# Performance work log

Measured on AMD Instinct MI355X. Metric: run time of the kernel, lower is better.

The kernel has to match this reference:

```python
import jax, jax.numpy as jnp
import numpy as np

D = 4096          # in_features == out_features (scale broadcast requires square W)
TOKENS = 16384


def setup_inputs() -> dict:
    key = jax.random.key(0)
    kx, kq, ks, kb = jax.random.split(key, 4)
    x = jax.random.normal(kx, (TOKENS, D), dtype=jnp.float32)
    # int4 quantized weights in [-8, 7] (stored int8 in torch; int32 here is fine)
    qweight = jax.random.randint(kq, (D, D), -8, 8, dtype=jnp.int32)
    # per-channel scales: positive, realistic magnitude ~ max|W|/7
    scale = jax.random.uniform(ks, (D,), dtype=jnp.float32, minval=1e-3, maxval=2e-2)
    bias = jax.random.normal(kb, (D,), dtype=jnp.float32)
    return {"x": x, "qweight": qweight, "scale": scale, "bias": bias}


def reference(x, qweight, scale, bias):
    # Dequantize: W[i, j] = qW[i, j] * scale[i]  (scale.view(-1,1) in the source)
    W = qweight.astype(jnp.float32) * scale[:, None]   # [out, in]
    # F.linear(x, W, bias) = x @ W.T + bias
    return x @ W.T + bias                               # [tokens, out]
```

## Files before the change

### kernel.cpp

```cpp
#include <hip/hip_runtime.h>

typedef __attribute__((ext_vector_type(4))) int  i8x16;
typedef __attribute__((ext_vector_type(16))) int i32x16;
typedef __attribute__((ext_vector_type(8))) short bf16x8;
typedef __attribute__((ext_vector_type(8))) unsigned short ushort8;
typedef __attribute__((ext_vector_type(4))) float f32x4;

__device__ __forceinline__ unsigned short f32_to_bf16(float f) {
    union { float f; unsigned int u; } v;
    v.f = f;
    unsigned int r = v.u + (0x7fffu + ((v.u >> 16) & 1u));
    return (unsigned short)(r >> 16);
}

__device__ __forceinline__ void gload_lds16(const void* g, void* l) {
    __builtin_amdgcn_global_load_lds(
        (const __attribute__((address_space(1))) unsigned int*)g,
        (__attribute__((address_space(3))) unsigned int*)l, 16, 0, 0);
}

__global__ __launch_bounds__(256) void quantx_kernel(const float* __restrict__ x,
                                                     char* __restrict__ xq,
                                                     float* __restrict__ rs, int K) {
    const int row = blockIdx.x;
    const float4* xr = (const float4*)(x + (size_t)row * K);
    const int K4 = K >> 2;
    const int t = threadIdx.x;
    float am = 0.f;
    for (int i = t; i < K4; i += 256) {
        float4 v = xr[i];
        am = fmaxf(am, fmaxf(fmaxf(fabsf(v.x), fabsf(v.y)),
                             fmaxf(fabsf(v.z), fabsf(v.w))));
    }
    for (int off = 32; off; off >>= 1) am = fmaxf(am, __shfl_xor(am, off));
    __shared__ float ws[4];
    if ((t & 63) == 0) ws[t >> 6] = am;
    __syncthreads();
    am = fmaxf(fmaxf(ws[0], ws[1]), fmaxf(ws[2], ws[3]));
    const float inv = am > 0.f ? 127.f / am : 0.f;
    if (t == 0) rs[row] = am > 0.f ? am / 127.f : 0.f;
    int* dst = (int*)(xq + (size_t)row * K);
    for (int i = t; i < K4; i += 256) {
        float4 v = xr[i];
        int a = (int)rintf(v.x * inv), b = (int)rintf(v.y * inv);
        int c = (int)rintf(v.z * inv), d = (int)rintf(v.w * inv);
        dst[i] = (a & 255) | ((b & 255) << 8) | ((c & 255) << 16) | (d << 24);
    }
}

__global__ void convq_kernel(const int* __restrict__ q, char* __restrict__ qb, long n16) {
    long i = (long)blockIdx.x * blockDim.x + threadIdx.x;
    const long stride = (long)gridDim.x * blockDim.x;
    for (; i < n16; i += stride) {
        const int4* p = (const int4*)(q + i * 16);
        int4 a = p[0], b = p[1], c = p[2], d = p[3];
        int4 r;
        r.x = (a.x & 255) | ((a.y & 255) << 8) | ((a.z & 255) << 16) | (a.w << 24);
        r.y = (b.x & 255) | ((b.y & 255) << 8) | ((b.z & 255) << 16) | (b.w << 24);
        r.z = (c.x & 255) | ((c.y & 255) << 8) | ((c.z & 255) << 16) | (c.w << 24);
        r.w = (d.x & 255) | ((d.y & 255) << 8) | ((d.z & 255) << 16) | (d.w << 24);
        ((int4*)qb)[i] = r;
    }
}

__global__ __launch_bounds__(512, 2) void qgemm_i8_kernel(
    const char* __restrict__ A, const char* __restrict__ B,
    const float* __restrict__ rs, const float* __restrict__ scale,
    const float* __restrict__ bias, float* __restrict__ C, int M, int N, int K) {
    extern __shared__ char sm[];

    const int tid  = threadIdx.x;
    const int lane = tid & 63;
    const int w    = tid >> 6;
    const int wr   = w >> 2;
    const int wc   = w & 3;
    const int l31  = lane & 31;
    const int hi   = lane >> 5;
    const int swz7 = l31 & 7;

    const int nwg = gridDim.x;
    const int bid = blockIdx.x;
    const int swz = (bid & 7) * (nwg >> 3) + (bid >> 3);
    const int nbx = N >> 8;
    const int m0  = (swz / nbx) << 8;
    const int n0  = (swz % nbx) << 8;

    const size_t binv0 = (size_t)(tid >> 3) * K +
                         (size_t)(((tid & 7) ^ ((tid >> 3) & 7)) << 4);
    const size_t bofs = (size_t)64 * K;
    const int bld = w << 10;

#define STAGE(LBASE, GSRC) do {                                       \
        gload_lds16((GSRC) + binv0,          (LBASE) + bld);          \
        gload_lds16((GSRC) + binv0 + bofs,   (LBASE) + bld + 8192);   \
        gload_lds16((GSRC) + binv0 + 2*bofs, (LBASE) + bld + 16384);  \
        gload_lds16((GSRC) + binv0 + 3*bofs, (LBASE) + bld + 24576); } while (0)

    const int aRow0 = (wr * 128 + l31) * 128;
    const int bRow0 = (wc * 64 + l31) * 128;

    const char* pA = A + (size_t)m0 * K;
    const char* pB = B + (size_t)n0 * K;
    const int NT = K >> 7;

    i32x16 acc[4][2];
#pragma unroll
    for (int mf = 0; mf < 4; ++mf)
#pragma unroll
        for (int nf = 0; nf < 2; ++nf)
#pragma unroll
            for (int r = 0; r < 16; ++r) acc[mf][nf][r] = 0;

#define RD_KH(BUFA, BUFB, KH) do {                                             \
    _Pragma("unroll") for (int mf = 0; mf < 4; ++mf)                           \
    _Pragma("unroll") for (int s = 0; s < 2; ++s)                              \
        aF[mf][s] = *(const i8x16*)((BUFA) + aRow0 + mf * 4096 +               \
            ((((KH) * 4 + s * 2 + hi) ^ swz7) << 4));                          \
    _Pragma("unroll") for (int nf = 0; nf < 2; ++nf)                           \
    _Pragma("unroll") for (int s = 0; s < 2; ++s)                              \
        bF[nf][s] = *(const i8x16*)((BUFB) + bRow0 + nf * 4096 +               \
            ((((KH) * 4 + s * 2 + hi) ^ swz7) << 4)); } while (0)
#define MFMA_KH() do {                                                         \
    _Pragma("unroll") for (int s = 0; s < 2; ++s)                              \
    _Pragma("unroll") for (int mf = 0; mf < 4; ++mf)                           \
    _Pragma("unroll") for (int nf = 0; nf < 2; ++nf)                           \
        acc[mf][nf] = __builtin_amdgcn_mfma_i32_32x32x32_i8(                   \
            aF[mf][s], bF[nf][s], acc[mf][nf], 0, 0, 0); } while (0)
#define LGKM0() do { asm volatile("s_waitcnt lgkmcnt(0)" ::: "memory");        \
                     __builtin_amdgcn_sched_barrier(0); } while (0)

    i8x16 aF[4][2], bF[2][2];

    STAGE(sm + 0,     pA);
    STAGE(sm + 65536, pB);
    if (NT > 1) {
        STAGE(sm + 32768, pA + 128);
        STAGE(sm + 98304, pB + 128);
        asm volatile("s_waitcnt vmcnt(8)" ::: "memory");
    } else {
        asm volatile("s_waitcnt vmcnt(0)" ::: "memory");
    }
    __builtin_amdgcn_s_barrier();

    for (int t = 0; t < NT; ++t) {
        char* Ac = sm + (t & 1) * 32768;
        char* Bc = sm + 65536 + (t & 1) * 32768;

        RD_KH(Ac, Bc, 0);
        LGKM0();
        __builtin_amdgcn_s_setprio(1);
        MFMA_KH();
        __builtin_amdgcn_s_setprio(0);

        RD_KH(Ac, Bc, 1);
        LGKM0();
        __builtin_amdgcn_s_setprio(1);
        MFMA_KH();
        __builtin_amdgcn_s_setprio(0);

        if (t + 1 < NT) {
            __builtin_amdgcn_s_barrier();
            if (t + 2 < NT) {
                STAGE(Ac, pA + (size_t)(t + 2) * 128);
                STAGE(Bc, pB + (size_t)(t + 2) * 128);
                asm volatile("s_waitcnt vmcnt(8)" ::: "memory");
            } else {
                asm volatile("s_waitcnt vmcnt(0)" ::: "memory");
            }
            __builtin_amdgcn_s_barrier();
        }
    }

#pragma unroll
    for (int mf = 0; mf < 4; ++mf) {
        const int rbase = m0 + wr * 128 + mf * 32 + 4 * hi;
#pragma unroll
        for (int nf = 0; nf < 2; ++nf) {
            const int col = n0 + wc * 64 + nf * 32 + l31;
            const float sc = scale[col];
            const float bs = bias[col];
#pragma unroll
            for (int reg = 0; reg < 16; ++reg) {
                const int row = rbase + 8 * (reg >> 2) + (reg & 3);
                C[(size_t)row * N + col] =
                    (float)acc[mf][nf][reg] * (rs[row] * sc) + bs;
            }
        }
    }
#undef STAGE
#undef RD_KH
#undef MFMA_KH
#undef LGKM0
}

__global__ __launch_bounds__(256) void qgemm_fb_kernel(
    const float* __restrict__ Af, const int* __restrict__ Bi,
    const float* __restrict__ scale, const float* __restrict__ bias,
    float* __restrict__ C, int M, int N, int K) {
    constexpr int BK = 64;
    __shared__ unsigned short lA[128 * BK];
    __shared__ unsigned short lB[128 * BK];
    const int t = threadIdx.x, lane = t & 63, w = t >> 6;
    const int wr = w >> 1, wc = w & 1;
    const int m0 = blockIdx.y * 128, n0 = blockIdx.x * 128;
    const int l15 = lane & 15, l4 = lane >> 4;
    f32x4 acc[4][4];
#pragma unroll
    for (int m = 0; m < 4; ++m)
#pragma unroll
        for (int n = 0; n < 4; ++n) acc[m][n] = (f32x4){0.f, 0.f, 0.f, 0.f};
    for (int k0 = 0; k0 < K; k0 += BK) {
        __syncthreads();
#pragma unroll
        for (int i = 0; i < 4; ++i) {
            const int off = i * 4096 + w * 1024 + lane * 16;
            const int row = off >> 7;
            const int col = (off & 127) >> 1;
            const float* pa = Af + (size_t)(m0 + row) * K + k0 + col;
            float4 a0 = *(const float4*)pa;
            float4 a1 = *(const float4*)(pa + 4);
            ushort8 va;
            va[0] = f32_to_bf16(a0.x); va[1] = f32_to_bf16(a0.y);
            va[2] = f32_to_bf16(a0.z); va[3] = f32_to_bf16(a0.w);
            va[4] = f32_to_bf16(a1.x); va[5] = f32_to_bf16(a1.y);
            va[6] = f32_to_bf16(a1.z); va[7] = f32_to_bf16(a1.w);
            *(ushort8*)((char*)lA + off) = va;
            const int* pb = Bi + (size_t)(n0 + row) * K + k0 + col;
            int4 b0 = *(const int4*)pb;
            int4 b1 = *(const int4*)(pb + 4);
            ushort8 vb;
            vb[0] = f32_to_bf16((float)b0.x); vb[1] = f32_to_bf16((float)b0.y);
            vb[2] = f32_to_bf16((float)b0.z); vb[3] = f32_to_bf16((float)b0.w);
            vb[4] = f32_to_bf16((float)b1.x); vb[5] = f32_to_bf16((float)b1.y);
            vb[6] = f32_to_bf16((float)b1.z); vb[7] = f32_to_bf16((float)b1.w);
            *(ushort8*)((char*)lB + off) = vb;
        }
        __syncthreads();
#pragma unroll
        for (int kk = 0; kk < BK; kk += 32) {
            bf16x8 af[4], bfr[4];
#pragma unroll
            for (int m = 0; m < 4; ++m)
                af[m] = *(const bf16x8*)&lA[(wr * 64 + m * 16 + l15) * BK + kk + l4 * 8];
#pragma unroll
            for (int n = 0; n < 4; ++n)
                bfr[n] = *(const bf16x8*)&lB[(wc * 64 + n * 16 + l15) * BK + kk + l4 * 8];
#pragma unroll
            for (int m = 0; m < 4; ++m)
#pragma unroll
                for (int n = 0; n < 4; ++n)
                    acc[m][n] = __builtin_amdgcn_mfma_f32_16x16x32_bf16(
                        af[m], bfr[n], acc[m][n], 0, 0, 0);
        }
    }
#pragma unroll
    for (int n = 0; n < 4; ++n) {
        const int col = n0 + wc * 64 + n * 16 + l15;
        const float sc = scale[col], bs = bias[col];
#pragma unroll
        for (int m = 0; m < 4; ++m) {
            const int row0 = m0 + wr * 64 + m * 16 + l4 * 4;
#pragma unroll
            for (int j = 0; j < 4; ++j)
                C[(size_t)(row0 + j) * N + col] = fmaf(acc[m][n][j], sc, bs);
        }
    }
}

extern "C" void kernel_launch(void* const* d_in, const int* in_sizes, int n_in,
                              void* d_out, int out_size, void* d_ws, size_t ws_size,
                              hipStream_t stream) {
    const float* x     = (const float*)d_in[0];
    const int*   q     = (const int*)d_in[1];
    const float* scale = (const float*)d_in[2];
    const float* bias  = (const float*)d_in[3];
    float*       out   = (float*)d_out;

    const int K = in_sizes[2];
    const int N = in_sizes[1] / K;
    const int M = in_sizes[0] / K;

    const size_t xq_b = (size_t)M * K;
    const size_t qb_b = (size_t)N * K;
    const size_t need = xq_b + qb_b + (size_t)M * 4;
    const int nwg = (M / 256) * (N / 256);

    if (ws_size >= need && (M % 256) == 0 && (N % 256) == 0 &&
        (K % 128) == 0 && K >= 256 && (nwg % 8) == 0) {
        char*  xq = (char*)d_ws;
        char*  qb = xq + xq_b;
        float* rs = (float*)(qb + qb_b);
        quantx_kernel<<<M, 256, 0, stream>>>(x, xq, rs, K);
        convq_kernel<<<2048, 256, 0, stream>>>(q, qb, (long)(qb_b / 16));
        qgemm_i8_kernel<<<nwg, 512, 131072, stream>>>(xq, qb, rs, scale, bias,
                                                      out, M, N, K);
    } else {
        dim3 grid(N / 128, M / 128);
        qgemm_fb_kernel<<<grid, 256, 0, stream>>>(x, q, scale, bias, out, M, N, K);
    }
}
```

Measured before the change: 413.3 us.

## Switch int8 GEMM to 256x128 tiles with 16x16x64 MFMA and smaller LDS

```diff
diff --git a/kernel.cpp b/kernel.cpp
--- a/kernel.cpp
+++ b/kernel.cpp
@@ -1,7 +1,7 @@
 #include <hip/hip_runtime.h>
 
 typedef __attribute__((ext_vector_type(4))) int  i8x16;
-typedef __attribute__((ext_vector_type(16))) int i32x16;
+typedef __attribute__((ext_vector_type(4))) int  i32x4;
 typedef __attribute__((ext_vector_type(8))) short bf16x8;
 typedef __attribute__((ext_vector_type(8))) unsigned short ushort8;
 typedef __attribute__((ext_vector_type(4))) float f32x4;
@@ -63,7 +63,7 @@
     }
 }
 
-__global__ __launch_bounds__(512, 2) void qgemm_i8_kernel(
+__global__ __launch_bounds__(512, 4) void qgemm_i8_kernel(
     const char* __restrict__ A, const char* __restrict__ B,
     const float* __restrict__ rs, const float* __restrict__ scale,
     const float* __restrict__ bias, float* __restrict__ C, int M, int N, int K) {
@@ -72,98 +72,78 @@
     const int tid  = threadIdx.x;
     const int lane = tid & 63;
     const int w    = tid >> 6;
-    const int wr   = w >> 2;
-    const int wc   = w & 3;
-    const int l31  = lane & 31;
-    const int hi   = lane >> 5;
-    const int swz7 = l31 & 7;
+    const int wr   = w >> 1;
+    const int wc   = w & 1;
+    const int l15  = lane & 15;
+    const int l4   = lane >> 4;
 
     const int nwg = gridDim.x;
     const int bid = blockIdx.x;
     const int swz = (bid & 7) * (nwg >> 3) + (bid >> 3);
-    const int nbx = N >> 8;
-    const int m0  = (swz / nbx) << 8;
-    const int n0  = (swz % nbx) << 8;
-
-    const size_t binv0 = (size_t)(tid >> 3) * K +
-                         (size_t)(((tid & 7) ^ ((tid >> 3) & 7)) << 4);
-    const size_t bofs = (size_t)64 * K;
-    const int bld = w << 10;
-
-#define STAGE(LBASE, GSRC) do {                                       \
-        gload_lds16((GSRC) + binv0,          (LBASE) + bld);          \
-        gload_lds16((GSRC) + binv0 + bofs,   (LBASE) + bld + 8192);   \
-        gload_lds16((GSRC) + binv0 + 2*bofs, (LBASE) + bld + 16384);  \
-        gload_lds16((GSRC) + binv0 + 3*bofs, (LBASE) + bld + 24576); } while (0)
-
-    const int aRow0 = (wr * 128 + l31) * 128;
-    const int bRow0 = (wc * 64 + l31) * 128;
+    const int nbn = N >> 7;
+    const int m0  = (swz / nbn) << 8;
+    const int n0  = (swz % nbn) << 7;
+
+    const size_t srcO = (size_t)(tid >> 2) * K +
+                        (size_t)(((tid & 3) ^ ((tid >> 2) & 3)) << 4);
+    const int ldsO = w << 10;
 
     const char* pA = A + (size_t)m0 * K;
     const char* pB = B + (size_t)n0 * K;
-    const int NT = K >> 7;
-
-    i32x16 acc[4][2];
+    const size_t hK = (size_t)128 * K;
+    const int NT = K >> 6;
+
+#define STAGE(Ab, Bb, kt) do {                                   \
+        gload_lds16(pA + srcO + (size_t)(kt) * 64, (Ab) + ldsO); \
+        gload_lds16(pA + srcO + hK + (size_t)(kt) * 64, (Ab) + ldsO + 8192); \
+        gload_lds16(pB + srcO + (size_t)(kt) * 64, (Bb) + ldsO); } while (0)
+
+    const int slot  = (l4 ^ (l15 & 3)) << 4;
+    const int aBase = (wr * 64 + l15) * 64 + slot;
+    const int bBase = (wc * 64 + l15) * 64 + slot;
+
+    i32x4 acc[4][4];
 #pragma unroll
     for (int mf = 0; mf < 4; ++mf)
 #pragma unroll
-        for (int nf = 0; nf < 2; ++nf)
-#pragma unroll
-            for (int r = 0; r < 16; ++r) acc[mf][nf][r] = 0;
-
-#define RD_KH(BUFA, BUFB, KH) do {                                             \
-    _Pragma("unroll") for (int mf = 0; mf < 4; ++mf)                           \
-    _Pragma("unroll") for (int s = 0; s < 2; ++s)                              \
-        aF[mf][s] = *(const i8x16*)((BUFA) + aRow0 + mf * 4096 +               \
-            ((((KH) * 4 + s * 2 + hi) ^ swz7) << 4));                          \
-    _Pragma("unroll") for (int nf = 0; nf < 2; ++nf)                           \
-    _Pragma("unroll") for (int s = 0; s < 2; ++s)                              \
-        bF[nf][s] = *(const i8x16*)((BUFB) + bRow0 + nf * 4096 +               \
-            ((((KH) * 4 + s * 2 + hi) ^ swz7) << 4)); } while (0)
-#define MFMA_KH() do {                                                         \
-    _Pragma("unroll") for (int s = 0; s < 2; ++s)                              \
-    _Pragma("unroll") for (int mf = 0; mf < 4; ++mf)                           \
-    _Pragma("unroll") for (int nf = 0; nf < 2; ++nf)                           \
-        acc[mf][nf] = __builtin_amdgcn_mfma_i32_32x32x32_i8(                   \
-            aF[mf][s], bF[nf][s], acc[mf][nf], 0, 0, 0); } while (0)
-#define LGKM0() do { asm volatile("s_waitcnt lgkmcnt(0)" ::: "memory");        \
-                     __builtin_amdgcn_sched_barrier(0); } while (0)
-
-    i8x16 aF[4][2], bF[2][2];
-
-    STAGE(sm + 0,     pA);
-    STAGE(sm + 65536, pB);
+        for (int nf = 0; nf < 4; ++nf) acc[mf][nf] = (i32x4){0, 0, 0, 0};
+
+    STAGE(sm + 0, sm + 32768, 0);
     if (NT > 1) {
-        STAGE(sm + 32768, pA + 128);
-        STAGE(sm + 98304, pB + 128);
-        asm volatile("s_waitcnt vmcnt(8)" ::: "memory");
+        STAGE(sm + 16384, sm + 40960, 1);
+        asm volatile("s_waitcnt vmcnt(3)" ::: "memory");
     } else {
         asm volatile("s_waitcnt vmcnt(0)" ::: "memory");
     }
     __builtin_amdgcn_s_barrier();
 
     for (int t = 0; t < NT; ++t) {
-        char* Ac = sm + (t & 1) * 32768;
-        char* Bc = sm + 65536 + (t & 1) * 32768;
-
-        RD_KH(Ac, Bc, 0);
-        LGKM0();
+        char* Ab = sm + (t & 1) * 16384;
+        char* Bb = sm + 32768 + (t & 1) * 8192;
+
+        i8x16 aF[4], bF[4];
+#pragma unroll
+        for (int mf = 0; mf < 4; ++mf)
+            aF[mf] = *(const i8x16*)(Ab + aBase + mf * 1024);
+#pragma unroll
+        for (int nf = 0; nf < 4; ++nf)
+            bF[nf] = *(const i8x16*)(Bb + bBase + nf * 1024);
+        asm volatile("s_waitcnt lgkmcnt(0)" ::: "memory");
+        __builtin_amdgcn_sched_barrier(0);
         __builtin_amdgcn_s_setprio(1);
-        MFMA_KH();
-        __builtin_amdgcn_s_setprio(0);
-
-        RD_KH(Ac, Bc, 1);
-        LGKM0();
-        __builtin_amdgcn_s_setprio(1);
-        MFMA_KH();
+#pragma unroll
+        for (int mf = 0; mf < 4; ++mf)
+#pragma unroll
+            for (int nf = 0; nf < 4; ++nf)
+                acc[mf][nf] = __builtin_amdgcn_mfma_i32_16x16x64_i8(
+                    aF[mf], bF[nf], acc[mf][nf], 0, 0, 0);
         __builtin_amdgcn_s_setprio(0);
 
         if (t + 1 < NT) {
             __builtin_amdgcn_s_barrier();
             if (t + 2 < NT) {
-                STAGE(Ac, pA + (size_t)(t + 2) * 128);
-                STAGE(Bc, pB + (size_t)(t + 2) * 128);
-                asm volatile("s_waitcnt vmcnt(8)" ::: "memory");
+                STAGE(Ab, Bb, t + 2);
+                asm volatile("s_waitcnt vmcnt(3)" ::: "memory");
             } else {
                 asm volatile("s_waitcnt vmcnt(0)" ::: "memory");
             }
@@ -173,24 +153,22 @@
 
 #pragma unroll
     for (int mf = 0; mf < 4; ++mf) {
-        const int rbase = m0 + wr * 128 + mf * 32 + 4 * hi;
-#pragma unroll
-        for (int nf = 0; nf < 2; ++nf) {
-            const int col = n0 + wc * 64 + nf * 32 + l31;
+        const int row0 = m0 + wr * 64 + mf * 16 + l4 * 4;
+        float rsv[4];
+#pragma unroll
+        for (int j = 0; j < 4; ++j) rsv[j] = rs[row0 + j];
+#pragma unroll
+        for (int nf = 0; nf < 4; ++nf) {
+            const int col = n0 + wc * 64 + nf * 16 + l15;
             const float sc = scale[col];
             const float bs = bias[col];
 #pragma unroll
-            for (int reg = 0; reg < 16; ++reg) {
-                const int row = rbase + 8 * (reg >> 2) + (reg & 3);
-                C[(size_t)row * N + col] =
-                    (float)acc[mf][nf][reg] * (rs[row] * sc) + bs;
-            }
+            for (int j = 0; j < 4; ++j)
+                C[(size_t)(row0 + j) * N + col] =
+                    (float)acc[mf][nf][j] * (rsv[j] * sc) + bs;
         }
     }
 #undef STAGE
-#undef RD_KH
-#undef MFMA_KH
-#undef LGKM0
 }
 
 __global__ __launch_bounds__(256) void qgemm_fb_kernel(
@@ -283,17 +261,17 @@
     const size_t xq_b = (size_t)M * K;
     const size_t qb_b = (size_t)N * K;
     const size_t need = xq_b + qb_b + (size_t)M * 4;
-    const int nwg = (M / 256) * (N / 256);
-
-    if (ws_size >= need && (M % 256) == 0 && (N % 256) == 0 &&
-        (K % 128) == 0 && K >= 256 && (nwg % 8) == 0) {
+    const int nwg = (M / 256) * (N / 128);
+
+    if (ws_size >= need && (M % 256) == 0 && (N % 128) == 0 &&
+        (K % 64) == 0 && K >= 128 && (nwg % 8) == 0) {
         char*  xq = (char*)d_ws;
         char*  qb = xq + xq_b;
         float* rs = (float*)(qb + qb_b);
         quantx_kernel<<<M, 256, 0, stream>>>(x, xq, rs, K);
         convq_kernel<<<2048, 256, 0, stream>>>(q, qb, (long)(qb_b / 16));
-        qgemm_i8_kernel<<<nwg, 512, 131072, stream>>>(xq, qb, rs, scale, bias,
-                                                      out, M, N, K);
+        qgemm_i8_kernel<<<nwg, 512, 49152, stream>>>(xq, qb, rs, scale, bias,
+                                                     out, M, N, K);
     } else {
         dim3 grid(N / 128, M / 128);
         qgemm_fb_kernel<<<grid, 256, 0, stream>>>(x, q, scale, bias, out, M, N, K);
```

New measurement: 403.9 us. 1.02x faster.
